# Kernel optimization log

Hardware: AMD Instinct MI355X
Metric: run time of the kernel (lower is better)

The kernel has to match this reference:

```python
import jax, jax.numpy as jnp
import numpy as np

B, S, D = 2, 4096, 512   # batch, seq_len, hidden_dim
H, E = 8, 64             # n_heads, head_dim


def setup_inputs() -> dict:
    key = jax.random.key(0)
    ks = jax.random.split(key, 14)
    s = 0.02  # init scale
    return {
        "x":  jax.random.normal(ks[0], (B, S, D), dtype=jnp.float32),
        # stacked per-head projection weights, stored as [H, in, out]
        "wq": jax.random.normal(ks[1], (H, D, E), dtype=jnp.float32) * s,
        "bq": jax.random.normal(ks[2], (H, E), dtype=jnp.float32) * s,
        "wk": jax.random.normal(ks[3], (H, D, E), dtype=jnp.float32) * s,
        "bk": jax.random.normal(ks[4], (H, E), dtype=jnp.float32) * s,
        "wv": jax.random.normal(ks[5], (H, D, E), dtype=jnp.float32) * s,
        "bv": jax.random.normal(ks[6], (H, E), dtype=jnp.float32) * s,
        "wo": jax.random.normal(ks[7], (H, E, D), dtype=jnp.float32) * s,
        "bo": jax.random.normal(ks[8], (H, D), dtype=jnp.float32) * s,
        # MLP: Linear(D,D) -> ReLU -> Linear(D,D), stored as [in, out]
        "w1": jax.random.normal(ks[9], (D, D), dtype=jnp.float32) * s,
        "b1": jax.random.normal(ks[10], (D,), dtype=jnp.float32) * s,
        "w2": jax.random.normal(ks[11], (D, D), dtype=jnp.float32) * s,
        "b2": jax.random.normal(ks[12], (D,), dtype=jnp.float32) * s,
    }


def reference(x, wq, bq, wk, bk, wv, bv, wo, bo, w1, b1, w2, b2):
    # Per-head projections, batched over heads: [B, H, S, E]
    q = jnp.einsum('bsd,hde->bhse', x, wq) + bq[None, :, None, :]
    k = jnp.einsum('bsd,hde->bhse', x, wk) + bk[None, :, None, :]
    v = jnp.einsum('bsd,hde->bhse', x, wv) + bv[None, :, None, :]
    scale = 1.0 / jnp.sqrt(jnp.asarray(q.shape[-1], q.dtype))
    scores = jnp.einsum('bhse,bhte->bhst', q, k) * scale  # [B,H,S,S]
    A = jax.nn.softmax(scores, axis=-1)
    ctx = jnp.einsum('bhst,bhte->bhse', A, v)             # [B,H,S,E]
    # w_o per head then sum over heads (each head adds its bias once)
    y = jnp.einsum('bhse,hed->bsd', ctx, wo) + jnp.sum(bo, axis=0)
    # MLP
    h = jax.nn.relu(y @ w1 + b1)
    return h @ w2 + b2
```

## Files before the change

kernel.cpp:

```cpp
#include <hip/hip_runtime.h>
#include <math.h>

#define Bsz 2
#define Sq  4096
#define Dm  512
#define Hn  8
#define Eh  64

typedef unsigned short u16;
typedef __attribute__((ext_vector_type(8))) short bf16x8;
typedef __attribute__((ext_vector_type(4))) float f32x4;
typedef __attribute__((ext_vector_type(16))) float f32x16;
typedef __attribute__((ext_vector_type(4))) unsigned short u16x4;

#define KSCALE 0.18033688011112042f

__device__ __forceinline__ u16 f2bf(float f) {
    unsigned int u = __float_as_uint(f);
    u += 0x7FFFu + ((u >> 16) & 1u);
    return (u16)(u >> 16);
}

__device__ __forceinline__ float fast_exp2(float x) {
#if defined(__HIP_DEVICE_COMPILE__) && __has_builtin(__builtin_amdgcn_exp2f)
    return __builtin_amdgcn_exp2f(x);
#else
    return exp2f(x);
#endif
}

__device__ __forceinline__ f32x16 mfma_32x32x16(bf16x8 a, bf16x8 b, f32x16 c) {
#if defined(__HIP_DEVICE_COMPILE__)
    return __builtin_amdgcn_mfma_f32_32x32x16_bf16(a, b, c, 0, 0, 0);
#else
    (void)a; (void)b;
    return c;
#endif
}

__device__ __forceinline__ unsigned cvt_pk_bf16(float lo, float hi) {
#if defined(__HIP_DEVICE_COMPILE__)
    unsigned r;
    asm("v_cvt_pk_bf16_f32 %0, %1, %2" : "=v"(r) : "v"(lo), "v"(hi));
    return r;
#else
    return ((unsigned)f2bf(hi) << 16) | (unsigned)f2bf(lo);
#endif
}

__device__ __forceinline__ void plane32_swap(unsigned &a, unsigned &b) {
#if defined(__HIP_DEVICE_COMPILE__)
    asm volatile("v_permlane32_swap_b32 %0, %1" : "+v"(a), "+v"(b));
#endif
}

__device__ __forceinline__ bf16x8 frag_of(unsigned a, unsigned b, unsigned c, unsigned d) {
    union { unsigned u[4]; bf16x8 v; } r;
    r.u[0] = a; r.u[1] = b; r.u[2] = c; r.u[3] = d;
    return r.v;
}

__device__ __forceinline__ void async16(const u16* g, u16* l) {
    __builtin_amdgcn_global_load_lds(
        (const __attribute__((address_space(1))) void*)g,
        (__attribute__((address_space(3))) void*)l, 16, 0, 0);
}

template<int TN, int NT>
__device__ __forceinline__ void gemm_core(
    const u16* __restrict__ A, const u16* __restrict__ WT,
    int m0, int n0, u16* Ast, u16* Bst, f32x4 (&acc)[4][NT])
{
    const int tid  = threadIdx.x;
    const int lane = tid & 63, wid = tid >> 6;
    const int l15  = lane & 15, quad = lane >> 4;
    const int wm = wid >> 1, wn = wid & 1;

    for (int kt = 0; kt < Dm / 64; ++kt) {
        const int k0 = kt * 64;
        __syncthreads();
#pragma unroll
        for (int j = 0; j < 4; ++j) {
            int ci = wid * 256 + j * 64 + lane;
            int row = ci >> 3, c = (ci & 7) ^ (row & 7);
            async16(&A[(size_t)(m0 + row) * Dm + k0 + c * 8],
                    &Ast[(size_t)(wid * 256 + j * 64) * 8]);
        }
#pragma unroll
        for (int j = 0; j < TN / 32; ++j) {
            int ci = wid * (TN * 2) + j * 64 + lane;
            int row = ci >> 3, c = (ci & 7) ^ (row & 7);
            async16(&WT[(size_t)(n0 + row) * Dm + k0 + c * 8],
                    &Bst[(size_t)(wid * (TN * 2) + j * 64) * 8]);
        }
        __syncthreads();
#pragma unroll
        for (int ks = 0; ks < 2; ++ks) {
            bf16x8 af[4], bfr[NT];
#pragma unroll
            for (int mt = 0; mt < 4; ++mt) {
                int r = wm * 64 + mt * 16 + l15;
                af[mt] = *(const bf16x8*)&Ast[(r * 8 + ((ks * 4 + quad) ^ (r & 7))) * 8];
            }
#pragma unroll
            for (int nt = 0; nt < NT; ++nt) {
                int n = wn * (TN / 2) + nt * 16 + l15;
                bfr[nt] = *(const bf16x8*)&Bst[(n * 8 + ((ks * 4 + quad) ^ (n & 7))) * 8];
            }
#pragma unroll
            for (int mt = 0; mt < 4; ++mt)
#pragma unroll
                for (int nt = 0; nt < NT; ++nt)
                    acc[mt][nt] = __builtin_amdgcn_mfma_f32_16x16x32_bf16(
                        af[mt], bfr[nt], acc[mt][nt], 0, 0, 0);
        }
    }
}

__global__ __launch_bounds__(256) void prep_kernel(
    const float* __restrict__ x,
    const float* __restrict__ wq, const float* __restrict__ wk,
    const float* __restrict__ wv, const float* __restrict__ wo,
    const float* __restrict__ w1, const float* __restrict__ w2,
    const float* __restrict__ bo,
    u16* __restrict__ xb, u16* __restrict__ wqkvT, u16* __restrict__ woT,
    u16* __restrict__ w1T, u16* __restrict__ w2T, float* __restrict__ bo_s)
{
    const int seg = blockIdx.y, bx = blockIdx.x, tid = threadIdx.x;
    if (seg == 0) {
        const float4* xi = (const float4*)x;
        const int stride = gridDim.x * 256;
        for (int i = bx * 256 + tid; i < (Bsz * Sq * Dm) / 4; i += stride) {
            float4 v = xi[i];
            u16x4 o = {f2bf(v.x), f2bf(v.y), f2bf(v.z), f2bf(v.w)};
            *(u16x4*)&xb[(size_t)i * 4] = o;
        }
        return;
    }
    if (seg == 7) {
        int d = bx * 256 + tid;
        if (d < Dm) {
            float s = 0.0f;
#pragma unroll
            for (int h = 0; h < Hn; ++h) s += bo[h * Dm + d];
            bo_s[d] = s;
        }
        return;
    }
    if (bx >= 64) return;
    __shared__ float t[64][65];
    const float* src; u16* dst; int ld_in;
    if (seg <= 3) {
        const float* w = (seg == 1) ? wq : (seg == 2) ? wk : wv;
        int head = bx >> 3, kt = bx & 7;
        src = w + (size_t)head * Dm * Eh + (size_t)kt * 64 * 64;
        ld_in = 64;
        dst = wqkvT + ((size_t)((seg - 1) * 8 + head) * 64) * 512 + kt * 64;
    } else {
        const float* w = (seg == 4) ? wo : (seg == 5) ? w1 : w2;
        u16* dT = (seg == 4) ? woT : (seg == 5) ? w1T : w2T;
        int tr = bx >> 3, tc = bx & 7;
        src = w + (size_t)(tr * 64) * 512 + tc * 64;
        ld_in = 512;
        dst = dT + (size_t)(tc * 64) * 512 + tr * 64;
    }
#pragma unroll
    for (int it = 0; it < 16; ++it) {
        int idx = it * 256 + tid;
        int r = idx >> 6, c = idx & 63;
        t[r][c] = src[(size_t)r * ld_in + c];
    }
    __syncthreads();
#pragma unroll
    for (int it = 0; it < 4; ++it) {
        int idx = it * 256 + tid;
        int oc = idx >> 4, og = idx & 15;
        u16x4 o;
#pragma unroll
        for (int j = 0; j < 4; ++j) o[j] = f2bf(t[og * 4 + j][oc]);
        *(u16x4*)&dst[(size_t)oc * 512 + og * 4] = o;
    }
}

__global__ __launch_bounds__(256, 2) void qkv_gemm(
    const u16* __restrict__ xb, const u16* __restrict__ wqkvT,
    const float* __restrict__ bq, const float* __restrict__ bk,
    const float* __restrict__ bv,
    u16* __restrict__ qb, u16* __restrict__ kb, u16* __restrict__ vbT)
{
    __shared__ __align__(16) u16 Ast[128 * 64];
    __shared__ __align__(16) u16 Bst[64 * 64];
    const int proj = blockIdx.y >> 3, h = blockIdx.y & 7;
    const u16* WT = wqkvT + (size_t)blockIdx.y * 64 * 512;

    f32x4 acc[4][2];
#pragma unroll
    for (int i = 0; i < 4; ++i)
#pragma unroll
        for (int j = 0; j < 2; ++j) acc[i][j] = (f32x4)0.0f;

    gemm_core<64, 2>(xb, WT, blockIdx.x * 128, 0, Ast, Bst, acc);

    const int tid = threadIdx.x;
    const int lane = tid & 63, wid = tid >> 6;
    const int l15 = lane & 15, quad = lane >> 4;
    const int wm = wid >> 1, wn = wid & 1;
    const float* bias = (proj == 0) ? bq : (proj == 1) ? bk : bv;

    const int mbase = blockIdx.x * 128 + wm * 64;
    const int b = mbase >> 12;
    const int sbase = (mbase & (Sq - 1));
    const int bh = b * Hn + h;

#pragma unroll
    for (int mt = 0; mt < 4; ++mt)
#pragma unroll
        for (int nt = 0; nt < 2; ++nt) {
            int e = wn * 32 + nt * 16 + l15;
            float bval = bias[h * Eh + e];
            int s = sbase + mt * 16 + quad * 4;
            if (proj == 2) {
                u16x4 o;
#pragma unroll
                for (int r = 0; r < 4; ++r) o[r] = f2bf(acc[mt][nt][r] + bval);
                *(u16x4*)&vbT[((size_t)bh * Eh + e) * Sq + s] = o;
            } else if (proj == 1) {
                for (int r = 0; r < 4; ++r)
                    kb[((size_t)bh * Sq + s + r) * Eh + e] =
                        f2bf((acc[mt][nt][r] + bval) * KSCALE);
            } else {
                for (int r = 0; r < 4; ++r)
                    qb[((size_t)bh * Sq + s + r) * Eh + e] = f2bf(acc[mt][nt][r] + bval);
            }
        }
}

__global__ __launch_bounds__(512, 4) void attn_kernel(
    const u16* __restrict__ qb, const u16* __restrict__ kb,
    const u16* __restrict__ vbT, u16* __restrict__ ctxb)
{
    __shared__ __align__(16) u16 kst[2][128 * 64];
    __shared__ __align__(16) u16 vst[2][64 * 128];

    const int tid  = threadIdx.x;
    const int lane = tid & 63, wid = tid >> 6;
    const int wq = wid & 3, wt = wid >> 2;
    const int l31  = lane & 31, hh = lane >> 5;
    const int bh = blockIdx.y;
    const int q0 = blockIdx.x * 128;
    const int b = bh >> 3, h = bh & 7;

    const u16* qg = qb + (size_t)bh * Sq * Eh;
    const u16* kg = kb + (size_t)bh * Sq * Eh;
    const u16* vg = vbT + (size_t)bh * Eh * Sq;

    int krow[2], kcol[2], vrow[2], vcol[2];
#pragma unroll
    for (int j = 0; j < 2; ++j) {
        int ci = wid * 128 + j * 64 + lane;
        krow[j] = ci >> 3;
        kcol[j] = (ci & 7) ^ (krow[j] & 7);
        vrow[j] = ci >> 4;
        int vc  = ci & 15;
        vcol[j] = (vc & 8) | ((vc & 7) ^ (vrow[j] & 7));
    }

    bf16x8 qf[4];
    {
        const u16* qrow = &qg[(size_t)(q0 + wq * 32 + l31) * Eh + hh * 8];
#pragma unroll
        for (int ks = 0; ks < 4; ++ks)
            qf[ks] = *(const bf16x8*)&qrow[ks * 16];
    }

    bf16x8 ones;
    {
        union { unsigned u[4]; bf16x8 v; } t;
        t.u[0] = t.u[1] = t.u[2] = t.u[3] = 0x3F803F80u;
        ones = t.v;
    }

    f32x16 O[2], lsum;
    O[0] = (f32x16)0.0f;
    O[1] = (f32x16)0.0f;
    lsum = (f32x16)0.0f;

    const int t7 = l31 & 7;
    const int tt0 = wt * 2, tt1 = tt0 + 1;
    const int trow0 = (tt0 * 32 + l31) * 64;
    const int trow1 = (tt1 * 32 + l31) * 64;

    auto issueT = [&](int kt, int buf) {
        const int t1 = kt * 128;
#pragma unroll
        for (int j = 0; j < 2; ++j) {
            async16(&kg[(size_t)(t1 + krow[j]) * Eh + kcol[j] * 8],
                    &kst[buf][(wid * 128 + j * 64) * 8]);
            async16(&vg[(size_t)vrow[j] * Sq + t1 + vcol[j] * 8],
                    &vst[buf][(wid * 128 + j * 64) * 8]);
        }
    };

    auto compute_tile = [&](int bu) {
        const u16* kcur = kst[bu];
        const u16* vcur = vst[bu];
        f32x16 S0 = (f32x16)0.0f, S1 = (f32x16)0.0f;

        __builtin_amdgcn_s_setprio(1);
#pragma unroll
        for (int ks = 0; ks < 4; ++ks) {
            bf16x8 kf = *(const bf16x8*)&kcur[trow0 + ((ks * 2 + hh) ^ t7) * 8];
            S0 = mfma_32x32x16(kf, qf[ks], S0);
        }
#pragma unroll
        for (int ks = 0; ks < 4; ++ks) {
            bf16x8 kf = *(const bf16x8*)&kcur[trow1 + ((ks * 2 + hh) ^ t7) * 8];
            S1 = mfma_32x32x16(kf, qf[ks], S1);
        }
        __builtin_amdgcn_s_setprio(0);

        unsigned pa[8];
#pragma unroll
        for (int j = 0; j < 8; ++j) {
            float p0 = fast_exp2(S0[2 * j]);
            float p1 = fast_exp2(S0[2 * j + 1]);
            pa[j] = cvt_pk_bf16(p0, p1);
        }
        plane32_swap(pa[0], pa[2]); plane32_swap(pa[1], pa[3]);
        plane32_swap(pa[4], pa[6]); plane32_swap(pa[5], pa[7]);
        bf16x8 f0a = frag_of(pa[0], pa[1], pa[2], pa[3]);
        bf16x8 f1a = frag_of(pa[4], pa[5], pa[6], pa[7]);

        __builtin_amdgcn_s_setprio(1);
        lsum = mfma_32x32x16(ones, f0a, lsum);
        lsum = mfma_32x32x16(ones, f1a, lsum);
#pragma unroll
        for (int et = 0; et < 2; ++et) {
            const int erow = (et * 32 + l31) * 128;
            int c0 = tt0 * 4 + hh, c1 = c0 + 2;
            int g0 = (c0 & 8) | ((c0 & 7) ^ t7);
            int g1 = (c1 & 8) | ((c1 & 7) ^ t7);
            bf16x8 v0 = *(const bf16x8*)&vcur[erow + g0 * 8];
            bf16x8 v1 = *(const bf16x8*)&vcur[erow + g1 * 8];
            O[et] = mfma_32x32x16(v0, f0a, O[et]);
            O[et] = mfma_32x32x16(v1, f1a, O[et]);
        }
        __builtin_amdgcn_s_setprio(0);

        unsigned pb[8];
#pragma unroll
        for (int j = 0; j < 8; ++j) {
            float p0 = fast_exp2(S1[2 * j]);
            float p1 = fast_exp2(S1[2 * j + 1]);
            pb[j] = cvt_pk_bf16(p0, p1);
        }
        plane32_swap(pb[0], pb[2]); plane32_swap(pb[1], pb[3]);
        plane32_swap(pb[4], pb[6]); plane32_swap(pb[5], pb[7]);
        bf16x8 f0b = frag_of(pb[0], pb[1], pb[2], pb[3]);
        bf16x8 f1b = frag_of(pb[4], pb[5], pb[6], pb[7]);

        __builtin_amdgcn_s_setprio(1);
        lsum = mfma_32x32x16(ones, f0b, lsum);
        lsum = mfma_32x32x16(ones, f1b, lsum);
#pragma unroll
        for (int et = 0; et < 2; ++et) {
            const int erow = (et * 32 + l31) * 128;
            int c0 = tt1 * 4 + hh, c1 = c0 + 2;
            int g0 = (c0 & 8) | ((c0 & 7) ^ t7);
            int g1 = (c1 & 8) | ((c1 & 7) ^ t7);
            bf16x8 v0 = *(const bf16x8*)&vcur[erow + g0 * 8];
            bf16x8 v1 = *(const bf16x8*)&vcur[erow + g1 * 8];
            O[et] = mfma_32x32x16(v0, f0b, O[et]);
            O[et] = mfma_32x32x16(v1, f1b, O[et]);
        }
        __builtin_amdgcn_s_setprio(0);
    };

    issueT(0, 0);
    for (int kt = 0; kt < Sq / 128; ++kt) {
        const int cur = kt & 1;
        __syncthreads();
        if (kt < Sq / 128 - 1) issueT(kt + 1, cur ^ 1);
        compute_tile(cur);
    }

    __syncthreads();
    float* redO = (float*)&kst[0][0];
    float* redL = (float*)&vst[0][0];
    const int rbase = (wq * 64 + lane) * 32;
    if (wt == 1) {
#pragma unroll
        for (int et = 0; et < 2; ++et)
#pragma unroll
            for (int c = 0; c < 4; ++c) {
                f32x4 v4;
#pragma unroll
                for (int i = 0; i < 4; ++i) v4[i] = O[et][c * 4 + i];
                *(f32x4*)&redO[rbase + (((et * 4 + c) ^ (lane & 7)) * 4)] = v4;
            }
        redL[wq * 64 + lane] = lsum[0];
    }
    __syncthreads();
    if (wt == 0) {
#pragma unroll
        for (int et = 0; et < 2; ++et)
#pragma unroll
            for (int c = 0; c < 4; ++c) {
                f32x4 v4 = *(const f32x4*)&redO[rbase + (((et * 4 + c) ^ (lane & 7)) * 4)];
#pragma unroll
                for (int i = 0; i < 4; ++i) O[et][c * 4 + i] += v4[i];
            }
        const float lp = lsum[0] + redL[wq * 64 + lane];
        const float rl = 1.0f / lp;

        const int qglob = q0 + wq * 32 + l31;
        u16* crow = ctxb + ((size_t)(b * Sq + qglob) * Hn + h) * Eh;
#pragma unroll
        for (int et = 0; et < 2; ++et)
#pragma unroll
            for (int g = 0; g < 4; ++g) {
                u16x4 o;
#pragma unroll
                for (int i = 0; i < 4; ++i) o[i] = f2bf(O[et][g * 4 + i] * rl);
                *(u16x4*)&crow[et * 32 + g * 8 + hh * 4] = o;
            }
    }
}

template<int MODE>
__global__ __launch_bounds__(256, 2) void gemmMN(
    const u16* __restrict__ A, const u16* __restrict__ WT,
    const float* __restrict__ bias, void* __restrict__ Cout)
{
    __shared__ __align__(16) u16 Ast[128 * 64];
    __shared__ __align__(16) u16 Bst[64 * 64];

    f32x4 acc[4][2];
#pragma unroll
    for (int i = 0; i < 4; ++i)
#pragma unroll
        for (int j = 0; j < 2; ++j) acc[i][j] = (f32x4)0.0f;

    gemm_core<64, 2>(A, WT, blockIdx.x * 128, blockIdx.y * 64, Ast, Bst, acc);

    const int tid = threadIdx.x;
    const int lane = tid & 63, wid = tid >> 6;
    const int l15 = lane & 15, quad = lane >> 4;
    const int m0 = blockIdx.x * 128 + (wid >> 1) * 64;
    const int n0 = blockIdx.y * 64 + (wid & 1) * 32;

#pragma unroll
    for (int mt = 0; mt < 4; ++mt)
#pragma unroll
        for (int nt = 0; nt < 2; ++nt) {
            int col = n0 + nt * 16 + l15;
            float bval = bias[col];
#pragma unroll
            for (int r = 0; r < 4; ++r) {
                int row = m0 + mt * 16 + quad * 4 + r;
                float v = acc[mt][nt][r] + bval;
                if (MODE == 1) v = fmaxf(v, 0.0f);
                if (MODE == 2) ((float*)Cout)[(size_t)row * Dm + col] = v;
                else           ((u16*)Cout)[(size_t)row * Dm + col] = f2bf(v);
            }
        }
}

extern "C" void kernel_launch(void* const* d_in, const int* in_sizes, int n_in,
                              void* d_out, int out_size, void* d_ws, size_t ws_size,
                              hipStream_t stream)
{
    const float* x  = (const float*)d_in[0];
    const float* wq = (const float*)d_in[1];
    const float* bq = (const float*)d_in[2];
    const float* wk = (const float*)d_in[3];
    const float* bk = (const float*)d_in[4];
    const float* wv = (const float*)d_in[5];
    const float* bv = (const float*)d_in[6];
    const float* wo = (const float*)d_in[7];
    const float* bo = (const float*)d_in[8];
    const float* w1 = (const float*)d_in[9];
    const float* b1 = (const float*)d_in[10];
    const float* w2 = (const float*)d_in[11];
    const float* b2 = (const float*)d_in[12];
    float* out = (float*)d_out;
    char* wsb = (char*)d_ws;

    const size_t MB = 1u << 20;
    u16*   xb    = (u16*)(wsb + 0);
    u16*   qb    = (u16*)(wsb + 8 * MB);
    u16*   kb    = (u16*)(wsb + 16 * MB);
    u16*   vbT   = (u16*)(wsb + 24 * MB);
    u16*   ctxb  = (u16*)(wsb + 32 * MB);
    u16*   ybuf  = (u16*)(wsb + 40 * MB);
    u16*   h1    = (u16*)(wsb + 48 * MB);
    u16*   wqkvT = (u16*)(wsb + 56 * MB);
    u16*   woT   = (u16*)(wsb + 58 * MB);
    u16*   w1T   = (u16*)(wsb + 59 * MB);
    u16*   w2T   = (u16*)(wsb + 60 * MB);
    float* bo_s  = (float*)(wsb + 61 * MB);

    prep_kernel<<<dim3(128, 8), 256, 0, stream>>>(
        x, wq, wk, wv, wo, w1, w2, bo, xb, wqkvT, woT, w1T, w2T, bo_s);
    qkv_gemm<<<dim3(Sq * Bsz / 128, 24), 256, 0, stream>>>(
        xb, wqkvT, bq, bk, bv, qb, kb, vbT);
    attn_kernel<<<dim3(Sq / 128, Bsz * Hn), 512, 0, stream>>>(qb, kb, vbT, ctxb);
    gemmMN<0><<<dim3(Bsz * Sq / 128, Dm / 64), 256, 0, stream>>>(ctxb, woT, bo_s, ybuf);
    gemmMN<1><<<dim3(Bsz * Sq / 128, Dm / 64), 256, 0, stream>>>(ybuf, w1T, b1, h1);
    gemmMN<2><<<dim3(Bsz * Sq / 128, Dm / 64), 256, 0, stream>>>(h1, w2T, b2, out);
}
```

Measured before the change: 223.8 us.

## Double-buffer LDS tiles in shared GEMM core and raise MFMA priority

The shared GEMM core now keeps two LDS buffers per operand. It issues the async global-to-LDS loads for the next K tile before computing on the current one, and uses one barrier per iteration instead of two. Shared-memory use in the QKV and MLP/output GEMM kernels doubles, which may limit occupancy. It also wraps the MFMA block in s_setprio to favour matrix instructions over other waves. The attention kernel is unchanged, so only the projection and MLP GEMMs are affected.

```diff
diff --git a/kernel.cpp b/kernel.cpp
--- a/kernel.cpp
+++ b/kernel.cpp
@@ -75,45 +75,65 @@
     const int lane = tid & 63, wid = tid >> 6;
     const int l15  = lane & 15, quad = lane >> 4;
     const int wm = wid >> 1, wn = wid & 1;
-
-    for (int kt = 0; kt < Dm / 64; ++kt) {
+    constexpr int ABUF = 128 * 64;
+    constexpr int BBUF = TN * 64;
+
+    int arow[4], acol[4], brow[TN / 32], bcol[TN / 32];
+#pragma unroll
+    for (int j = 0; j < 4; ++j) {
+        int ci = wid * 256 + j * 64 + lane;
+        arow[j] = ci >> 3; acol[j] = (ci & 7) ^ (arow[j] & 7);
+    }
+#pragma unroll
+    for (int j = 0; j < TN / 32; ++j) {
+        int ci = wid * (TN * 2) + j * 64 + lane;
+        brow[j] = ci >> 3; bcol[j] = (ci & 7) ^ (brow[j] & 7);
+    }
+
+    auto issue = [&](int kt, int buf) {
         const int k0 = kt * 64;
-        __syncthreads();
-#pragma unroll
-        for (int j = 0; j < 4; ++j) {
-            int ci = wid * 256 + j * 64 + lane;
-            int row = ci >> 3, c = (ci & 7) ^ (row & 7);
-            async16(&A[(size_t)(m0 + row) * Dm + k0 + c * 8],
-                    &Ast[(size_t)(wid * 256 + j * 64) * 8]);
-        }
-#pragma unroll
-        for (int j = 0; j < TN / 32; ++j) {
-            int ci = wid * (TN * 2) + j * 64 + lane;
-            int row = ci >> 3, c = (ci & 7) ^ (row & 7);
-            async16(&WT[(size_t)(n0 + row) * Dm + k0 + c * 8],
-                    &Bst[(size_t)(wid * (TN * 2) + j * 64) * 8]);
-        }
-        __syncthreads();
+#pragma unroll
+        for (int j = 0; j < 4; ++j)
+            async16(&A[(size_t)(m0 + arow[j]) * Dm + k0 + acol[j] * 8],
+                    &Ast[buf * ABUF + (wid * 256 + j * 64) * 8]);
+#pragma unroll
+        for (int j = 0; j < TN / 32; ++j)
+            async16(&WT[(size_t)(n0 + brow[j]) * Dm + k0 + bcol[j] * 8],
+                    &Bst[buf * BBUF + (wid * (TN * 2) + j * 64) * 8]);
+    };
+
+    auto compute = [&](int buf) {
+        const u16* Ab = &Ast[buf * ABUF];
+        const u16* Bb = &Bst[buf * BBUF];
 #pragma unroll
         for (int ks = 0; ks < 2; ++ks) {
             bf16x8 af[4], bfr[NT];
 #pragma unroll
             for (int mt = 0; mt < 4; ++mt) {
                 int r = wm * 64 + mt * 16 + l15;
-                af[mt] = *(const bf16x8*)&Ast[(r * 8 + ((ks * 4 + quad) ^ (r & 7))) * 8];
+                af[mt] = *(const bf16x8*)&Ab[(r * 8 + ((ks * 4 + quad) ^ (r & 7))) * 8];
             }
 #pragma unroll
             for (int nt = 0; nt < NT; ++nt) {
                 int n = wn * (TN / 2) + nt * 16 + l15;
-                bfr[nt] = *(const bf16x8*)&Bst[(n * 8 + ((ks * 4 + quad) ^ (n & 7))) * 8];
-            }
+                bfr[nt] = *(const bf16x8*)&Bb[(n * 8 + ((ks * 4 + quad) ^ (n & 7))) * 8];
+            }
+            __builtin_amdgcn_s_setprio(1);
 #pragma unroll
             for (int mt = 0; mt < 4; ++mt)
 #pragma unroll
                 for (int nt = 0; nt < NT; ++nt)
                     acc[mt][nt] = __builtin_amdgcn_mfma_f32_16x16x32_bf16(
                         af[mt], bfr[nt], acc[mt][nt], 0, 0, 0);
-        }
+            __builtin_amdgcn_s_setprio(0);
+        }
+    };
+
+    issue(0, 0);
+    for (int kt = 0; kt < Dm / 64; ++kt) {
+        __syncthreads();
+        if (kt < Dm / 64 - 1) issue(kt + 1, (kt & 1) ^ 1);
+        compute(kt & 1);
     }
 }
 
@@ -188,8 +208,8 @@
     const float* __restrict__ bv,
     u16* __restrict__ qb, u16* __restrict__ kb, u16* __restrict__ vbT)
 {
-    __shared__ __align__(16) u16 Ast[128 * 64];
-    __shared__ __align__(16) u16 Bst[64 * 64];
+    __shared__ __align__(16) u16 Ast[2][128 * 64];
+    __shared__ __align__(16) u16 Bst[2][64 * 64];
     const int proj = blockIdx.y >> 3, h = blockIdx.y & 7;
     const u16* WT = wqkvT + (size_t)blockIdx.y * 64 * 512;
 
@@ -199,7 +219,7 @@
 #pragma unroll
         for (int j = 0; j < 2; ++j) acc[i][j] = (f32x4)0.0f;
 
-    gemm_core<64, 2>(xb, WT, blockIdx.x * 128, 0, Ast, Bst, acc);
+    gemm_core<64, 2>(xb, WT, blockIdx.x * 128, 0, &Ast[0][0], &Bst[0][0], acc);
 
     const int tid = threadIdx.x;
     const int lane = tid & 63, wid = tid >> 6;
@@ -432,8 +452,8 @@
     const u16* __restrict__ A, const u16* __restrict__ WT,
     const float* __restrict__ bias, void* __restrict__ Cout)
 {
-    __shared__ __align__(16) u16 Ast[128 * 64];
-    __shared__ __align__(16) u16 Bst[64 * 64];
+    __shared__ __align__(16) u16 Ast[2][128 * 64];
+    __shared__ __align__(16) u16 Bst[2][64 * 64];
 
     f32x4 acc[4][2];
 #pragma unroll
@@ -441,7 +461,8 @@
 #pragma unroll
         for (int j = 0; j < 2; ++j) acc[i][j] = (f32x4)0.0f;
 
-    gemm_core<64, 2>(A, WT, blockIdx.x * 128, blockIdx.y * 64, Ast, Bst, acc);
+    gemm_core<64, 2>(A, WT, blockIdx.x * 128, blockIdx.y * 64,
+                     &Ast[0][0], &Bst[0][0], acc);
 
     const int tid = threadIdx.x;
     const int lane = tid & 63, wid = tid >> 6;
```

Measured after the change: 231.3 us. 1.03x slower.

## Use 64x64 tiles with 32x32 MFMA for output/MLP GEMMs, add setprio

Applied to the files above, without the earlier changes.

Replaces the 128x64-tile gemmMN with a 64x64-tile variant where each wave computes a 32x32 block using 32x32x16 MFMA. This doubles the grid (256x8 blocks) and allows four blocks per CU, aimed at better occupancy and CU fill for the three 8192x512x512 GEMMs. It also wraps the MFMA sections, including those in the shared gemm_core used by the QKV GEMM, in s_setprio raises to favor matrix issue. The smaller tile lowers per-block data reuse and adds more global loads per FLOP.

```diff
diff --git a/kernel.cpp b/kernel.cpp
--- a/kernel.cpp
+++ b/kernel.cpp
@@ -107,12 +107,14 @@
                 int n = wn * (TN / 2) + nt * 16 + l15;
                 bfr[nt] = *(const bf16x8*)&Bst[(n * 8 + ((ks * 4 + quad) ^ (n & 7))) * 8];
             }
+            __builtin_amdgcn_s_setprio(1);
 #pragma unroll
             for (int mt = 0; mt < 4; ++mt)
 #pragma unroll
                 for (int nt = 0; nt < NT; ++nt)
                     acc[mt][nt] = __builtin_amdgcn_mfma_f32_16x16x32_bf16(
                         af[mt], bfr[nt], acc[mt][nt], 0, 0, 0);
+            __builtin_amdgcn_s_setprio(0);
         }
     }
 }
@@ -428,41 +430,64 @@
 }
 
 template<int MODE>
-__global__ __launch_bounds__(256, 2) void gemmMN(
+__global__ __launch_bounds__(256, 4) void gemmMN64(
     const u16* __restrict__ A, const u16* __restrict__ WT,
     const float* __restrict__ bias, void* __restrict__ Cout)
 {
-    __shared__ __align__(16) u16 Ast[128 * 64];
+    __shared__ __align__(16) u16 Ast[64 * 64];
     __shared__ __align__(16) u16 Bst[64 * 64];
 
-    f32x4 acc[4][2];
-#pragma unroll
-    for (int i = 0; i < 4; ++i)
-#pragma unroll
-        for (int j = 0; j < 2; ++j) acc[i][j] = (f32x4)0.0f;
-
-    gemm_core<64, 2>(A, WT, blockIdx.x * 128, blockIdx.y * 64, Ast, Bst, acc);
-
-    const int tid = threadIdx.x;
+    const int tid  = threadIdx.x;
     const int lane = tid & 63, wid = tid >> 6;
-    const int l15 = lane & 15, quad = lane >> 4;
-    const int m0 = blockIdx.x * 128 + (wid >> 1) * 64;
-    const int n0 = blockIdx.y * 64 + (wid & 1) * 32;
-
-#pragma unroll
-    for (int mt = 0; mt < 4; ++mt)
-#pragma unroll
-        for (int nt = 0; nt < 2; ++nt) {
-            int col = n0 + nt * 16 + l15;
-            float bval = bias[col];
-#pragma unroll
-            for (int r = 0; r < 4; ++r) {
-                int row = m0 + mt * 16 + quad * 4 + r;
-                float v = acc[mt][nt][r] + bval;
-                if (MODE == 1) v = fmaxf(v, 0.0f);
-                if (MODE == 2) ((float*)Cout)[(size_t)row * Dm + col] = v;
-                else           ((u16*)Cout)[(size_t)row * Dm + col] = f2bf(v);
-            }
+    const int l31  = lane & 31, hh = lane >> 5;
+    const int wm = wid >> 1, wn = wid & 1;
+    const int m0 = blockIdx.x * 64, n0 = blockIdx.y * 64;
+
+    int srow[2], scol[2];
+#pragma unroll
+    for (int j = 0; j < 2; ++j) {
+        int ci = wid * 128 + j * 64 + lane;
+        srow[j] = ci >> 3;
+        scol[j] = (ci & 7) ^ (srow[j] & 7);
+    }
+
+    f32x16 acc = (f32x16)0.0f;
+    const int ar = wm * 32 + l31;
+    const int br = wn * 32 + l31;
+    const int arx = ar & 7, brx = br & 7;
+
+    for (int kt = 0; kt < Dm / 64; ++kt) {
+        const int k0 = kt * 64;
+        __syncthreads();
+#pragma unroll
+        for (int j = 0; j < 2; ++j) {
+            async16(&A[(size_t)(m0 + srow[j]) * Dm + k0 + scol[j] * 8],
+                    &Ast[(wid * 128 + j * 64) * 8]);
+            async16(&WT[(size_t)(n0 + srow[j]) * Dm + k0 + scol[j] * 8],
+                    &Bst[(wid * 128 + j * 64) * 8]);
+        }
+        __syncthreads();
+        __builtin_amdgcn_s_setprio(1);
+#pragma unroll
+        for (int ks = 0; ks < 4; ++ks) {
+            bf16x8 af = *(const bf16x8*)&Ast[(ar * 8 + ((ks * 2 + hh) ^ arx)) * 8];
+            bf16x8 bf = *(const bf16x8*)&Bst[(br * 8 + ((ks * 2 + hh) ^ brx)) * 8];
+            acc = mfma_32x32x16(af, bf, acc);
+        }
+        __builtin_amdgcn_s_setprio(0);
+    }
+
+    const int col = n0 + wn * 32 + l31;
+    const float bval = bias[col];
+#pragma unroll
+    for (int g = 0; g < 4; ++g)
+#pragma unroll
+        for (int i = 0; i < 4; ++i) {
+            int row = m0 + wm * 32 + g * 8 + hh * 4 + i;
+            float v = acc[g * 4 + i] + bval;
+            if (MODE == 1) v = fmaxf(v, 0.0f);
+            if (MODE == 2) ((float*)Cout)[(size_t)row * Dm + col] = v;
+            else           ((u16*)Cout)[(size_t)row * Dm + col] = f2bf(v);
         }
 }
 
@@ -505,7 +530,7 @@
     qkv_gemm<<<dim3(Sq * Bsz / 128, 24), 256, 0, stream>>>(
         xb, wqkvT, bq, bk, bv, qb, kb, vbT);
     attn_kernel<<<dim3(Sq / 128, Bsz * Hn), 512, 0, stream>>>(qb, kb, vbT, ctxb);
-    gemmMN<0><<<dim3(Bsz * Sq / 128, Dm / 64), 256, 0, stream>>>(ctxb, woT, bo_s, ybuf);
-    gemmMN<1><<<dim3(Bsz * Sq / 128, Dm / 64), 256, 0, stream>>>(ybuf, w1T, b1, h1);
-    gemmMN<2><<<dim3(Bsz * Sq / 128, Dm / 64), 256, 0, stream>>>(h1, w2T, b2, out);
-}
+    gemmMN64<0><<<dim3(Bsz * Sq / 64, Dm / 64), 256, 0, stream>>>(ctxb, woT, bo_s, ybuf);
+    gemmMN64<1><<<dim3(Bsz * Sq / 64, Dm / 64), 256, 0, stream>>>(ybuf, w1T, b1, h1);
+    gemmMN64<2><<<dim3(Bsz * Sq / 64, Dm / 64), 256, 0, stream>>>(h1, w2T, b2, out);
+}
```

After: 230.0 us. +2.8%, slower.
